# Kernel tuning notes

Measured on AMD Instinct MI355X. Metric: run time of the kernel, lower is better.

Reference implementation:

```python
import jax, jax.numpy as jnp
import numpy as np

EMBED_DIM = 1024
LATENT = 512
HEADS = 8
HEAD_DIM = EMBED_DIM // HEADS        # 128
LAT_HD = LATENT // HEADS             # 64
EPS = 1e-5


def _layernorm(x, gamma, beta):
    mu = jnp.mean(x, axis=-1, keepdims=True)
    var = jnp.mean(jnp.square(x - mu), axis=-1, keepdims=True)
    return (x - mu) * jax.lax.rsqrt(var + EPS) * gamma + beta


def setup_inputs() -> dict:
    key = jax.random.key(0)
    ks = jax.random.split(key, 12)
    B, N, M = 8, 8192, 256
    s_in = 1.0 / np.sqrt(EMBED_DIM)
    return {
        "input_tokens": jax.random.normal(ks[0], (B, N, EMBED_DIM), jnp.float32),
        "query_tokens": jax.random.normal(ks[1], (B, M, EMBED_DIM), jnp.float32),
        # Linear weights stored as [in, out] so y = x @ W + b
        "q_w": jax.random.normal(ks[2], (EMBED_DIM, LATENT), jnp.float32) * s_in,
        "q_b": jnp.zeros((LATENT,), jnp.float32),
        "q_g": jnp.ones((LATENT,), jnp.float32),
        "q_beta": jnp.zeros((LATENT,), jnp.float32),
        "k_w": jax.random.normal(ks[3], (EMBED_DIM, LATENT), jnp.float32) * s_in,
        "k_b": jnp.zeros((LATENT,), jnp.float32),
        "k_g": jnp.ones((LATENT,), jnp.float32),
        "k_beta": jnp.zeros((LATENT,), jnp.float32),
        "v_w": jax.random.normal(ks[4], (EMBED_DIM, EMBED_DIM), jnp.float32) * s_in,
        "v_b": jnp.zeros((EMBED_DIM,), jnp.float32),
        "v_g": jnp.ones((EMBED_DIM,), jnp.float32),
        "v_beta": jnp.zeros((EMBED_DIM,), jnp.float32),
        "proj_w": jax.random.normal(ks[5], (EMBED_DIM, EMBED_DIM), jnp.float32) * s_in,
        "proj_b": jnp.zeros((EMBED_DIM,), jnp.float32),
    }


def reference(input_tokens, query_tokens, q_w, q_b, q_g, q_beta,
              k_w, k_b, k_g, k_beta, v_w, v_b, v_g, v_beta,
              proj_w, proj_b):
    B, N, C = input_tokens.shape
    M = query_tokens.shape[1]
    # projections + layernorms
    q = _layernorm(query_tokens @ q_w + q_b, q_g, q_beta)   # [B,M,LATENT]
    k = _layernorm(input_tokens @ k_w + k_b, k_g, k_beta)   # [B,N,LATENT]
    v = _layernorm(input_tokens @ v_w + v_b, v_g, v_beta)   # [B,N,C]
    # split heads: q,k -> [B,H,*,LAT_HD]; v -> [B,H,N,HEAD_DIM]
    q = q.reshape(B, M, HEADS, LAT_HD).transpose(0, 2, 1, 3)
    k = k.reshape(B, N, HEADS, LAT_HD).transpose(0, 2, 1, 3)
    v = v.reshape(B, N, HEADS, HEAD_DIM).transpose(0, 2, 1, 3)
    # softmax Q over latent head dim; softmax K^T over token dim N
    q = jax.nn.softmax(q, axis=-1)                 # [B,H,M,LAT_HD]
    kT = jax.nn.softmax(k.transpose(0, 1, 3, 2), axis=-1)  # [B,H,LAT_HD,N]
    kv = jnp.einsum('bhln,bhnd->bhld', kT, v)      # [B,H,LAT_HD,HEAD_DIM]
    out = jnp.einsum('bhml,bhld->bhmd', q, kv)     # [B,H,M,HEAD_DIM]
    out = out.transpose(0, 2, 1, 3).reshape(B, M, C)
    return out @ proj_w + proj_b
```

## Files before the change

### kernel.cpp

```cpp
#include <hip/hip_runtime.h>
#include <hip/hip_fp16.h>

typedef _Float16 f16;
typedef _Float16 f16x8 __attribute__((ext_vector_type(8)));
typedef _Float16 f16x4 __attribute__((ext_vector_type(4)));
typedef float f32x4 __attribute__((ext_vector_type(4)));

#define LN_EPS 1e-5f

typedef __attribute__((address_space(1))) unsigned int as1_u32;
typedef __attribute__((address_space(3))) unsigned int as3_u32;

__device__ __forceinline__ void gload_lds16(const void* g, void* l) {
    __builtin_amdgcn_global_load_lds((as1_u32*)g, (as3_u32*)l, 16, 0, 0);
}

__device__ __forceinline__ f32x4 mfma16(f16x8 a, f16x8 b, f32x4 c) {
    return __builtin_amdgcn_mfma_f32_16x16x32_f16(a, b, c, 0, 0, 0);
}


__global__ void k_cvt_dual(const float4* __restrict__ in0, const float4* __restrict__ in1,
                           f16x4* __restrict__ out0, f16x4* __restrict__ out1,
                           int nsplit, int ntot) {
    int i = blockIdx.x * blockDim.x + threadIdx.x;
    int st = gridDim.x * blockDim.x;
    for (; i < ntot; i += st) {
        const bool lo = i < nsplit;
        const float4 v = lo ? in0[i] : in1[i - nsplit];
        f16x4 o;
        o.x = (f16)v.x; o.y = (f16)v.y; o.z = (f16)v.z; o.w = (f16)v.w;
        if (lo) out0[i] = o; else out1[i - nsplit] = o;
    }
}

__global__ __launch_bounds__(256) void k_transpose_all(const float* __restrict__ kw,
                                                       const float* __restrict__ vw,
                                                       const float* __restrict__ qw,
                                                       const float* __restrict__ pw,
                                                       f16* __restrict__ BkvT,
                                                       f16* __restrict__ qwT,
                                                       f16* __restrict__ pwT) {
    __shared__ float t[32][33];
    const int x = blockIdx.x;
    const float* W; f16* WT; int Nw, nt0;
    if (x < 16)      { W = kw; WT = BkvT;                     Nw = 512;  nt0 = x; }
    else if (x < 48) { W = vw; WT = BkvT + (size_t)512 * 1024; Nw = 1024; nt0 = x - 16; }
    else if (x < 64) { W = qw; WT = qwT;                      Nw = 512;  nt0 = x - 48; }
    else             { W = pw; WT = pwT;                      Nw = 1024; nt0 = x - 64; }
    const int n0 = nt0 * 32, k0 = blockIdx.y * 32;
    const int tx = threadIdx.x & 31, ty = threadIdx.x >> 5;
#pragma unroll
    for (int i = 0; i < 32; i += 8)
        t[ty + i][tx] = W[(size_t)(k0 + ty + i) * Nw + n0 + tx];
    __syncthreads();
#pragma unroll
    for (int i = 0; i < 32; i += 8)
        WT[(size_t)(n0 + ty + i) * 1024 + k0 + tx] = (f16)t[tx][ty + i];
}


__global__ __launch_bounds__(512, 2) void k_gemm256(const f16* __restrict__ A,
                                                    const f16* __restrict__ Bt,
                                                    f16* __restrict__ C,
                                                    const float* __restrict__ bias1,
                                                    const float* __restrict__ bias2) {
    extern __shared__ char lds[];
    const int tid = threadIdx.x, lane = tid & 63, w = tid >> 6;
    const int wr = w >> 2, wc = w & 3;
    const int lane15 = lane & 15, l4 = lane >> 4;

    const int swz = ((int)blockIdx.x & 7) * 192 + ((int)blockIdx.x >> 3);
    const int bx = swz % 6, by = swz / 6;
    const size_t m0 = (size_t)by * 256, n0g = (size_t)bx * 256;

    const int lrow = lane >> 3;
    const int slot = (lane & 7) ^ lrow;
    const int rw = w * 32;
    const f16* gA = A + (m0 + rw + lrow) * 1024 + slot * 8;
    const f16* gB = Bt + (n0g + rw + lrow) * 1024 + slot * 8;
    const int ldsw = rw * 128;

    const int sf = l4 ^ (lane15 & 7);
    const int offA = (wr * 128 + lane15) * 128 + sf * 16;
    const int offB = (wc * 64 + lane15) * 128 + sf * 16;

    f32x4 acc[8][4] = {};

#define STAGE(t, bsel)                                                          \
    {                                                                           \
        const int k0s = (t) * 64;                                               \
        char* dA = lds + ((bsel) << 15) + ldsw;                                 \
        char* dB = lds + 65536 + ((bsel) << 15) + ldsw;                         \
        _Pragma("unroll")                                                       \
        for (int i = 0; i < 4; i++) {                                           \
            gload_lds16(gA + (size_t)i * 8192 + k0s, dA + i * 1024);            \
            gload_lds16(gB + (size_t)i * 8192 + k0s, dB + i * 1024);            \
        }                                                                       \
    }

    STAGE(0, 0)
    STAGE(1, 1)
    asm volatile("s_waitcnt vmcnt(8)" ::: "memory");
    __builtin_amdgcn_s_barrier();

    for (int t = 0; t < 16; ++t) {
        const int bsel = t & 1;
        const char* pA = lds + (bsel << 15);
        const char* pB = lds + 65536 + (bsel << 15);
#pragma unroll
        for (int q = 0; q < 4; ++q) {
            const int mh = (q >> 1) * 4, nh = (q & 1) * 2;
            f16x8 af[4][2], bf[2][2];
#pragma unroll
            for (int mi = 0; mi < 4; mi++)
#pragma unroll
                for (int kk = 0; kk < 2; kk++)
                    af[mi][kk] = *(const f16x8*)(pA + ((offA + (mh + mi) * 2048) ^ (kk << 6)));
#pragma unroll
            for (int ni = 0; ni < 2; ni++)
#pragma unroll
                for (int kk = 0; kk < 2; kk++)
                    bf[ni][kk] = *(const f16x8*)(pB + ((offB + (nh + ni) * 2048) ^ (kk << 6)));
            __builtin_amdgcn_s_setprio(1);
#pragma unroll
            for (int mi = 0; mi < 4; mi++)
#pragma unroll
                for (int ni = 0; ni < 2; ni++)
#pragma unroll
                    for (int kk = 0; kk < 2; kk++)
                        acc[mh + mi][nh + ni] =
                            mfma16(af[mi][kk], bf[ni][kk], acc[mh + mi][nh + ni]);
            __builtin_amdgcn_s_setprio(0);
        }
        __builtin_amdgcn_s_barrier();
        if (t < 14) {
            STAGE(t + 2, bsel)
            asm volatile("s_waitcnt vmcnt(8)" ::: "memory");
        } else {
            asm volatile("s_waitcnt vmcnt(0)" ::: "memory");
        }
        __builtin_amdgcn_s_barrier();
    }
#undef STAGE

    {
        f16* Ct = (f16*)lds;
#pragma unroll
        for (int mi = 0; mi < 8; mi++) {
#pragma unroll
            for (int ni = 0; ni < 4; ni++) {
                const int row = wr * 128 + mi * 16 + l4 * 4;
                const int col = wc * 64 + ni * 16 + lane15;
                const int cg = (int)n0g + col;
                const float bv = (cg < 512) ? bias1[cg] : bias2[cg - 512];
#pragma unroll
                for (int j = 0; j < 4; j++)
                    Ct[(row + j) * 256 + col] = (f16)(acc[mi][ni][j] + bv);
            }
        }
        asm volatile("s_waitcnt lgkmcnt(0)" ::: "memory");
        __builtin_amdgcn_s_barrier();
#pragma unroll
        for (int it = 0; it < 16; it++) {
            const int flat = it * 512 + tid;
            const int row = flat >> 5;
            const int ce = (flat & 31) * 8;
            *(f16x8*)(C + (m0 + row) * 1536 + n0g + ce) = *(const f16x8*)(Ct + row * 256 + ce);
        }
    }
}


template <bool OUTF32>
__global__ __launch_bounds__(256, 2) void k_gemm(const f16* __restrict__ A,
                                                 const f16* __restrict__ Bt,
                                                 void* __restrict__ Cout, int Ncols, int Kd,
                                                 const float* __restrict__ bias1,
                                                 const float* __restrict__ bias2, int bsplit) {
    __shared__ f16 smem[16384];
    const int tid = threadIdx.x, lane = tid & 63, wave = tid >> 6;
    const int m0 = blockIdx.y * 128, n0 = blockIdx.x * 128;
    const size_t ldb = (size_t)Kd * 2;
    f32x4 acc[4][4] = {};

    const int rA = wave * 8 + (lane >> 3);
    const int slot = (lane & 7) * 16;
    const char* Ab = (const char*)A + (size_t)(m0 + rA) * ldb + slot;
    const char* Bb = (const char*)Bt + (size_t)(n0 + rA) * ldb + slot;
    char* lA = (char*)smem + wave * 1024;
    char* lB = (char*)smem + 16384 + wave * 1024;

    const int wm = (wave & 1) * 64, wn = (wave >> 1) * 64;

    for (int k0 = 0; k0 < Kd; k0 += 64) {
#pragma unroll
        for (int i = 0; i < 4; i++) {
            gload_lds16(Ab + (size_t)k0 * 2 + (size_t)i * 32 * ldb, lA + i * 4096);
            gload_lds16(Bb + (size_t)k0 * 2 + (size_t)i * 32 * ldb, lB + i * 4096);
        }
        __syncthreads();
#pragma unroll
        for (int kk = 0; kk < 64; kk += 32) {
            const int kb = (kk + (lane >> 4) * 8) * 2;
            f16x8 af[4], bf[4];
#pragma unroll
            for (int mi = 0; mi < 4; mi++)
                af[mi] = *(const f16x8*)((const char*)smem + (wm + mi * 16 + (lane & 15)) * 128 + kb);
#pragma unroll
            for (int ni = 0; ni < 4; ni++)
                bf[ni] = *(const f16x8*)((const char*)smem + 16384 + (wn + ni * 16 + (lane & 15)) * 128 + kb);
#pragma unroll
            for (int mi = 0; mi < 4; mi++)
#pragma unroll
                for (int ni = 0; ni < 4; ni++)
                    acc[mi][ni] = mfma16(af[mi], bf[ni], acc[mi][ni]);
        }
        __syncthreads();
    }

    if (!OUTF32) {
        f16* Ct = smem;
#pragma unroll
        for (int mi = 0; mi < 4; mi++) {
#pragma unroll
            for (int ni = 0; ni < 4; ni++) {
                const int r = wm + mi * 16 + (lane >> 4) * 4;
                const int c = wn + ni * 16 + (lane & 15);
                const int cg = n0 + c;
                const float bv = (cg < bsplit) ? bias1[cg] : bias2[cg - bsplit];
#pragma unroll
                for (int j = 0; j < 4; j++) Ct[(r + j) * 128 + c] = (f16)(acc[mi][ni][j] + bv);
            }
        }
        __syncthreads();
        f16* Cg = (f16*)Cout;
        const int r = tid >> 1, half = tid & 1;
        const f16* src = Ct + r * 128 + half * 64;
        f16* dst = Cg + (size_t)(m0 + r) * Ncols + n0 + half * 64;
#pragma unroll
        for (int i = 0; i < 8; i++) *(f16x8*)(dst + i * 8) = *(const f16x8*)(src + i * 8);
    } else {
        float* Cg = (float*)Cout;
#pragma unroll
        for (int mi = 0; mi < 4; mi++) {
#pragma unroll
            for (int ni = 0; ni < 4; ni++) {
                const int r = wm + mi * 16 + (lane >> 4) * 4;
                const int c = wn + ni * 16 + (lane & 15);
                const int cg = n0 + c;
                const float bv = (cg < bsplit) ? bias1[cg] : bias2[cg - bsplit];
#pragma unroll
                for (int j = 0; j < 4; j++)
                    Cg[(size_t)(m0 + r + j) * Ncols + cg] = acc[mi][ni][j] + bv;
            }
        }
    }
}


__global__ __launch_bounds__(192) void k_rowstats(const f16* __restrict__ Ckv,
                                                  float* __restrict__ stats) {
    const int row = blockIdx.x, t = threadIdx.x;
    const f16x8 v = ((const f16x8*)(Ckv + (size_t)row * 1536))[t];
    float s = 0.f, s2 = 0.f;
#pragma unroll
    for (int j = 0; j < 8; j++) {
        float x = (float)v[j];
        s += x;
        s2 += x * x;
    }
#pragma unroll
    for (int off = 32; off; off >>= 1) {
        s += __shfl_xor(s, off);
        s2 += __shfl_xor(s2, off);
    }
    __shared__ float red[4];
    const int wave = t >> 6;
    if ((t & 63) == 0 && wave) {
        red[wave * 2 - 2] = s;
        red[wave * 2 - 1] = s2;
    }
    __syncthreads();
    float* st = stats + (size_t)row * 4;
    if (t == 0) {
        const float mu = s * (1.0f / 512.0f);
        const float var = s2 * (1.0f / 512.0f) - mu * mu;
        st[0] = mu;
        st[1] = rsqrtf(var + LN_EPS);
    } else if (t == 64) {
        const float ss = s + red[2], ss2 = s2 + red[3];
        const float mu = ss * (1.0f / 1024.0f);
        const float var = ss2 * (1.0f / 1024.0f) - mu * mu;
        st[2] = mu;
        st[3] = rsqrtf(var + LN_EPS);
    }
}


__global__ __launch_bounds__(256) void k_colstats1(const f16* __restrict__ Ckv,
                                                   const float4* __restrict__ stats,
                                                   const float* __restrict__ kg,
                                                   const float* __restrict__ kb,
                                                   float* __restrict__ pm, float* __restrict__ ps) {
    const int b = blockIdx.y, slab = blockIdx.x, t = threadIdx.x;
    const int c0 = t * 2;
    const float g0 = kg[c0], g1 = kg[c0 + 1], e0 = kb[c0], e1 = kb[c0 + 1];
    const size_t r0 = (size_t)b * 8192 + slab * 64;
    float m0 = -1e30f, m1 = -1e30f;
    for (int r = 0; r < 64; r++) {
        const float4 st = stats[r0 + r];
        union { unsigned u; f16 h[2]; } w;
        w.u = *(const unsigned*)(Ckv + (r0 + r) * 1536 + c0);
        const float z0 = ((float)w.h[0] - st.x) * st.y * g0 + e0;
        const float z1 = ((float)w.h[1] - st.x) * st.y * g1 + e1;
        m0 = fmaxf(m0, z0);
        m1 = fmaxf(m1, z1);
    }
    float s0 = 0.f, s1 = 0.f;
    for (int r = 0; r < 64; r++) {
        const float4 st = stats[r0 + r];
        union { unsigned u; f16 h[2]; } w;
        w.u = *(const unsigned*)(Ckv + (r0 + r) * 1536 + c0);
        const float z0 = ((float)w.h[0] - st.x) * st.y * g0 + e0;
        const float z1 = ((float)w.h[1] - st.x) * st.y * g1 + e1;
        s0 += __expf(z0 - m0);
        s1 += __expf(z1 - m1);
    }
    const int o = (b * 128 + slab) * 512 + c0;
    pm[o] = m0; pm[o + 1] = m1;
    ps[o] = s0; ps[o + 1] = s1;
}

__global__ void k_colstats2(const float* __restrict__ pm, const float* __restrict__ ps,
                            float* __restrict__ Mx, float* __restrict__ invZ) {
    const int idx = blockIdx.x * 256 + threadIdx.x;
    const int b = idx >> 9, c = idx & 511;
    float M = -1e30f;
    for (int s = 0; s < 128; s++) M = fmaxf(M, pm[(b * 128 + s) * 512 + c]);
    float S = 0.f;
    for (int s = 0; s < 128; s++) S += ps[(b * 128 + s) * 512 + c] * __expf(pm[(b * 128 + s) * 512 + c] - M);
    Mx[idx] = M;
    invZ[idx] = 1.0f / S;
}


__global__ __launch_bounds__(256, 2) void k_kv(const f16* __restrict__ Ckv,
                                               const float4* __restrict__ stats,
                                               const float* __restrict__ kg,
                                               const float* __restrict__ kbe,
                                               const float* __restrict__ vg,
                                               const float* __restrict__ vbe,
                                               const float* __restrict__ Mx,
                                               float* __restrict__ kvpart) {
    __shared__ f16 As[64 * 64];
    __shared__ f16 Vs[128 * 64];
    __shared__ float cgk[64], cbk[64], cmx[64], cgv[128], cbv[128];
    const int split = blockIdx.x, bh = blockIdx.y;
    const int b = bh >> 3, h = bh & 7;
    const int tid = threadIdx.x, lane = tid & 63, wave = tid >> 6;
    if (tid < 64) {
        cgk[tid] = kg[h * 64 + tid];
        cbk[tid] = kbe[h * 64 + tid];
        cmx[tid] = Mx[b * 512 + h * 64 + tid];
    }
    if (tid < 128) {
        cgv[tid] = vg[h * 128 + tid];
        cbv[tid] = vbe[h * 128 + tid];
    }
    __syncthreads();
    f32x4 acc[8] = {};
    const size_t base = (size_t)b * 8192 + split * 1024;
    for (int t0 = 0; t0 < 1024; t0 += 64) {
        {
            const int g = tid & 7, p = tid >> 3;
            const size_t row = base + t0 + 2 * p;
            const f16x8 x0 = *(const f16x8*)(Ckv + row * 1536 + h * 64 + g * 8);
            const f16x8 x1 = *(const f16x8*)(Ckv + (row + 1) * 1536 + h * 64 + g * 8);
            const float4 s0 = stats[row], s1 = stats[row + 1];
#pragma unroll
            for (int j = 0; j < 8; j++) {
                const int c = g * 8 + j;
                const float z0 = ((float)x0[j] - s0.x) * s0.y * cgk[c] + cbk[c] - cmx[c];
                const float z1 = ((float)x1[j] - s1.x) * s1.y * cgk[c] + cbk[c] - cmx[c];
                union { unsigned u; f16 h2[2]; } pk;
                pk.h2[0] = (f16)__expf(z0);
                pk.h2[1] = (f16)__expf(z1);
                *(unsigned*)((char*)As + c * 128 + 4 * p) = pk.u;
            }
        }
#pragma unroll
        for (int sub = 0; sub < 2; sub++) {
            const int idx = tid + sub * 256;
            const int g = idx & 15, p = idx >> 4;
            const size_t row = base + t0 + 2 * p;
            const f16x8 x0 = *(const f16x8*)(Ckv + row * 1536 + 512 + h * 128 + g * 8);
            const f16x8 x1 = *(const f16x8*)(Ckv + (row + 1) * 1536 + 512 + h * 128 + g * 8);
            const float4 s0 = stats[row], s1 = stats[row + 1];
#pragma unroll
            for (int j = 0; j < 8; j++) {
                const int d = g * 8 + j;
                const float z0 = ((float)x0[j] - s0.z) * s0.w * cgv[d] + cbv[d];
                const float z1 = ((float)x1[j] - s1.z) * s1.w * cgv[d] + cbv[d];
                union { unsigned u; f16 h2[2]; } pk;
                pk.h2[0] = (f16)z0;
                pk.h2[1] = (f16)z1;
                *(unsigned*)((char*)Vs + d * 128 + 4 * p) = pk.u;
            }
        }
        __syncthreads();
#pragma unroll
        for (int kk = 0; kk < 64; kk += 32) {
            const int kb2 = (kk + (lane >> 4) * 8) * 2;
            const f16x8 af = *(const f16x8*)((const char*)As + (wave * 16 + (lane & 15)) * 128 + kb2);
#pragma unroll
            for (int ni = 0; ni < 8; ni++) {
                const f16x8 bf = *(const f16x8*)((const char*)Vs + (ni * 16 + (lane & 15)) * 128 + kb2);
                acc[ni] = mfma16(af, bf, acc[ni]);
            }
        }
        __syncthreads();
    }
    float* out = kvpart + ((size_t)split * 64 + bh) * 8192;
    const int l = wave * 16 + (lane >> 4) * 4;
#pragma unroll
    for (int ni = 0; ni < 8; ni++) {
        const int d = ni * 16 + (lane & 15);
#pragma unroll
        for (int j = 0; j < 4; j++) out[(l + j) * 128 + d] = acc[ni][j];
    }
}

__global__ void k_kvreduce(const float* __restrict__ kvpart, const float* __restrict__ invZ,
                           f16* __restrict__ kvT) {
    const int idx = blockIdx.x * 256 + threadIdx.x;
    const int d = idx & 127, l = (idx >> 7) & 63, bh = idx >> 13;
    const int b = bh >> 3, h = bh & 7;
    float s = 0.f;
#pragma unroll
    for (int sp = 0; sp < 8; sp++) s += kvpart[((size_t)sp * 64 + bh) * 8192 + l * 128 + d];
    s *= invZ[b * 512 + h * 64 + l];
    kvT[((size_t)bh * 128 + d) * 64 + l] = (f16)s;
}


__global__ __launch_bounds__(512) void k_qsm(const f16* __restrict__ qlin,
                                             const float* __restrict__ qg,
                                             const float* __restrict__ qbeta,
                                             f16* __restrict__ qsm) {
    const int row = blockIdx.x, t = threadIdx.x;
    const float x = (float)qlin[(size_t)row * 512 + t];
    float s = x, s2 = x * x;
#pragma unroll
    for (int off = 32; off; off >>= 1) {
        s += __shfl_xor(s, off);
        s2 += __shfl_xor(s2, off);
    }
    __shared__ float rs[16];
    const int wave = t >> 6, lane = t & 63;
    if (lane == 0) {
        rs[wave] = s;
        rs[8 + wave] = s2;
    }
    __syncthreads();
    float S = 0.f, S2 = 0.f;
#pragma unroll
    for (int w = 0; w < 8; w++) {
        S += rs[w];
        S2 += rs[8 + w];
    }
    const float mu = S * (1.0f / 512.0f);
    const float var = S2 * (1.0f / 512.0f) - mu * mu;
    const float z = (x - mu) * rsqrtf(var + LN_EPS) * qg[t] + qbeta[t];
    float m = z;
#pragma unroll
    for (int off = 32; off; off >>= 1) m = fmaxf(m, __shfl_xor(m, off));
    const float e = __expf(z - m);
    float se = e;
#pragma unroll
    for (int off = 32; off; off >>= 1) se += __shfl_xor(se, off);
    qsm[(size_t)row * 512 + t] = (f16)(e / se);
}


__global__ __launch_bounds__(256) void k_qkv(const f16* __restrict__ qsm,
                                             const f16* __restrict__ kvT,
                                             f16* __restrict__ omid) {
    const int ms = blockIdx.x, bh = blockIdx.y;
    const int b = bh >> 3, h = bh & 7;
    const int tid = threadIdx.x, lane = tid & 63, wave = tid >> 6;
    const int mr = ms * 64 + wave * 16;
    f32x4 acc[8] = {};
    const f16* Ab = qsm + (size_t)(b * 256 + mr + (lane & 15)) * 512 + h * 64;
    const f16* Bb = kvT + (size_t)bh * 8192;
#pragma unroll
    for (int kk = 0; kk < 64; kk += 32) {
        const int k = kk + (lane >> 4) * 8;
        const f16x8 af = *(const f16x8*)(Ab + k);
#pragma unroll
        for (int ni = 0; ni < 8; ni++) {
            const f16x8 bf = *(const f16x8*)(Bb + (ni * 16 + (lane & 15)) * 64 + k);
            acc[ni] = mfma16(af, bf, acc[ni]);
        }
    }
    const int r = b * 256 + mr + (lane >> 4) * 4;
#pragma unroll
    for (int ni = 0; ni < 8; ni++) {
        const int d = h * 128 + ni * 16 + (lane & 15);
#pragma unroll
        for (int j = 0; j < 4; j++) omid[(size_t)(r + j) * 1024 + d] = (f16)acc[ni][j];
    }
}


extern "C" void kernel_launch(void* const* d_in, const int* in_sizes, int n_in,
                              void* d_out, int out_size, void* d_ws, size_t ws_size,
                              hipStream_t stream) {
    const float* input  = (const float*)d_in[0];
    const float* query  = (const float*)d_in[1];
    const float* q_w    = (const float*)d_in[2];
    const float* q_b    = (const float*)d_in[3];
    const float* q_g    = (const float*)d_in[4];
    const float* q_beta = (const float*)d_in[5];
    const float* k_w    = (const float*)d_in[6];
    const float* k_b    = (const float*)d_in[7];
    const float* k_g    = (const float*)d_in[8];
    const float* k_beta = (const float*)d_in[9];
    const float* v_w    = (const float*)d_in[10];
    const float* v_b    = (const float*)d_in[11];
    const float* v_g    = (const float*)d_in[12];
    const float* v_beta = (const float*)d_in[13];
    const float* proj_w = (const float*)d_in[14];
    const float* proj_b = (const float*)d_in[15];

    char* ws = (char*)d_ws;
    size_t off = 0;
    auto alloc = [&](size_t bytes) {
        char* p = ws + off;
        off += (bytes + 255) & ~(size_t)255;
        return p;
    };
    f16*   A16    = (f16*)alloc((size_t)67108864 * 2);
    f16*   Q16    = (f16*)alloc((size_t)2097152 * 2);
    f16*   BkvT   = (f16*)alloc((size_t)1536 * 1024 * 2);
    f16*   qwT    = (f16*)alloc((size_t)512 * 1024 * 2);
    f16*   pwT    = (f16*)alloc((size_t)1024 * 1024 * 2);
    f16*   Ckv    = (f16*)alloc((size_t)65536 * 1536 * 2);
    float* stats  = (float*)alloc((size_t)65536 * 16);
    float* pm     = (float*)alloc((size_t)8 * 128 * 512 * 4);
    float* ps     = (float*)alloc((size_t)8 * 128 * 512 * 4);
    float* Mx     = (float*)alloc((size_t)8 * 512 * 4);
    float* invZ   = (float*)alloc((size_t)8 * 512 * 4);
    f16*   qlin   = (f16*)alloc((size_t)2048 * 512 * 2);
    f16*   qsm    = (f16*)alloc((size_t)2048 * 512 * 2);
    float* kvpart = (float*)alloc((size_t)8 * 64 * 64 * 128 * 4);
    f16*   kvT    = (f16*)alloc((size_t)64 * 128 * 64 * 2);
    f16*   omid   = (f16*)alloc((size_t)2048 * 1024 * 2);
    (void)ws_size; (void)in_sizes; (void)n_in; (void)out_size;

    hipFuncSetAttribute(reinterpret_cast<const void*>(k_gemm256),
                        hipFuncAttributeMaxDynamicSharedMemorySize, 131072);

    k_cvt_dual<<<2048, 256, 0, stream>>>((const float4*)input, (const float4*)query,
                                         (f16x4*)A16, (f16x4*)Q16, 16777216, 17301504);
    k_transpose_all<<<dim3(96, 32), 256, 0, stream>>>(k_w, v_w, q_w, proj_w, BkvT, qwT, pwT);

    k_gemm256<<<1536, 512, 131072, stream>>>(A16, BkvT, Ckv, k_b, v_b);

    k_rowstats<<<65536, 192, 0, stream>>>(Ckv, stats);

    k_colstats1<<<dim3(128, 8), 256, 0, stream>>>(Ckv, (const float4*)stats, k_g, k_beta, pm, ps);
    k_colstats2<<<16, 256, 0, stream>>>(pm, ps, Mx, invZ);

    k_kv<<<dim3(8, 64), 256, 0, stream>>>(Ckv, (const float4*)stats, k_g, k_beta, v_g, v_beta, Mx, kvpart);
    k_kvreduce<<<2048, 256, 0, stream>>>(kvpart, invZ, kvT);

    k_gemm<false><<<dim3(4, 16), 256, 0, stream>>>(Q16, qwT, qlin, 512, 1024, q_b, q_b, 512);
    k_qsm<<<2048, 512, 0, stream>>>(qlin, q_g, q_beta, qsm);
    k_qkv<<<dim3(4, 64), 256, 0, stream>>>(qsm, kvT, omid);
    k_gemm<true><<<dim3(8, 16), 256, 0, stream>>>(omid, pwT, d_out, 1024, 1024, proj_b, proj_b, 2048);
}
```

Baseline: 897.9 us.

## Fuse LayerNorm row stats into big GEMM epilogue and deepen K pipeline

```diff
diff --git a/kernel.cpp b/kernel.cpp
--- a/kernel.cpp
+++ b/kernel.cpp
@@ -64,7 +64,8 @@
                                                     const f16* __restrict__ Bt,
                                                     f16* __restrict__ C,
                                                     const float* __restrict__ bias1,
-                                                    const float* __restrict__ bias2) {
+                                                    const float* __restrict__ bias2,
+                                                    float* __restrict__ stats) {
     extern __shared__ char lds[];
     const int tid = threadIdx.x, lane = tid & 63, w = tid >> 6;
     const int wr = w >> 2, wc = w & 3;
@@ -74,93 +75,78 @@
     const int bx = swz % 6, by = swz / 6;
     const size_t m0 = (size_t)by * 256, n0g = (size_t)bx * 256;
 
-    const int lrow = lane >> 3;
-    const int slot = (lane & 7) ^ lrow;
-    const int rw = w * 32;
-    const f16* gA = A + (m0 + rw + lrow) * 1024 + slot * 8;
-    const f16* gB = Bt + (n0g + rw + lrow) * 1024 + slot * 8;
-    const int ldsw = rw * 128;
-
-    const int sf = l4 ^ (lane15 & 7);
-    const int offA = (wr * 128 + lane15) * 128 + sf * 16;
-    const int offB = (wc * 64 + lane15) * 128 + sf * 16;
+    const int lrow4 = lane >> 2;
+    const int lchunk = (lane & 3) ^ ((lane >> 3) & 3);
+    const f16* gA = A + (m0 + w * 32 + lrow4) * 1024 + lchunk * 8;
+    const f16* gB = Bt + (n0g + w * 32 + lrow4) * 1024 + lchunk * 8;
+    const int dstA = w * 2048;
+
+    const int csw = l4 ^ ((lane15 >> 1) & 3);
+    const int ofsA = (wr * 128 + lane15) * 64 + csw * 16;
+    const int ofsB = 16384 + (wc * 64 + lane15) * 64 + csw * 16;
 
     f32x4 acc[8][4] = {};
 
-#define STAGE(t, bsel)                                                          \
-    {                                                                           \
-        const int k0s = (t) * 64;                                               \
-        char* dA = lds + ((bsel) << 15) + ldsw;                                 \
-        char* dB = lds + 65536 + ((bsel) << 15) + ldsw;                         \
-        _Pragma("unroll")                                                       \
-        for (int i = 0; i < 4; i++) {                                           \
-            gload_lds16(gA + (size_t)i * 8192 + k0s, dA + i * 1024);            \
-            gload_lds16(gB + (size_t)i * 8192 + k0s, dB + i * 1024);            \
-        }                                                                       \
-    }
-
-    STAGE(0, 0)
-    STAGE(1, 1)
+#define STAGE_C(content)                                                         \
+    {                                                                            \
+        const int _sl = (content) & 3;                                           \
+        const int _ko = ((content) >> 1) * 64 + ((content) & 1) * 32;            \
+        char* _b = lds + _sl * 32768;                                            \
+        gload_lds16(gA + _ko, _b + dstA);                                        \
+        gload_lds16(gA + _ko + 16 * 1024, _b + dstA + 1024);                     \
+        gload_lds16(gB + _ko, _b + 16384 + dstA);                                \
+        gload_lds16(gB + _ko + 16 * 1024, _b + 16384 + dstA + 1024);             \
+    }
+
+#define PHASE(slotc, stage_content, vmN)                                         \
+    {                                                                            \
+        const char* sb = lds + (slotc) * 32768;                                  \
+        f16x8 af[8], bf[4];                                                      \
+        _Pragma("unroll") for (int m = 0; m < 8; m++)                            \
+            af[m] = *(const f16x8*)(sb + ofsA + m * 1024);                       \
+        _Pragma("unroll") for (int n = 0; n < 4; n++)                            \
+            bf[n] = *(const f16x8*)(sb + ofsB + n * 1024);                       \
+        if ((stage_content) >= 0) STAGE_C(stage_content)                         \
+        if ((vmN) == 8) asm volatile("s_waitcnt vmcnt(8)" ::: "memory");         \
+        else if ((vmN) == 4) asm volatile("s_waitcnt vmcnt(4)" ::: "memory");    \
+        else if ((vmN) == 0) asm volatile("s_waitcnt vmcnt(0)" ::: "memory");    \
+        __builtin_amdgcn_s_barrier();                                            \
+        __builtin_amdgcn_s_setprio(1);                                           \
+        _Pragma("unroll") for (int m = 0; m < 8; m++)                            \
+            _Pragma("unroll") for (int n = 0; n < 4; n++)                        \
+                acc[m][n] = mfma16(af[m], bf[n], acc[m][n]);                     \
+        __builtin_amdgcn_s_setprio(0);                                           \
+        __builtin_amdgcn_s_barrier();                                            \
+    }
+
+    STAGE_C(0) STAGE_C(1) STAGE_C(2)
     asm volatile("s_waitcnt vmcnt(8)" ::: "memory");
     __builtin_amdgcn_s_barrier();
 
-    for (int t = 0; t < 16; ++t) {
-        const int bsel = t & 1;
-        const char* pA = lds + (bsel << 15);
-        const char* pB = lds + 65536 + (bsel << 15);
-#pragma unroll
-        for (int q = 0; q < 4; ++q) {
-            const int mh = (q >> 1) * 4, nh = (q & 1) * 2;
-            f16x8 af[4][2], bf[2][2];
-#pragma unroll
-            for (int mi = 0; mi < 4; mi++)
-#pragma unroll
-                for (int kk = 0; kk < 2; kk++)
-                    af[mi][kk] = *(const f16x8*)(pA + ((offA + (mh + mi) * 2048) ^ (kk << 6)));
-#pragma unroll
-            for (int ni = 0; ni < 2; ni++)
-#pragma unroll
-                for (int kk = 0; kk < 2; kk++)
-                    bf[ni][kk] = *(const f16x8*)(pB + ((offB + (nh + ni) * 2048) ^ (kk << 6)));
-            __builtin_amdgcn_s_setprio(1);
-#pragma unroll
-            for (int mi = 0; mi < 4; mi++)
-#pragma unroll
-                for (int ni = 0; ni < 2; ni++)
-#pragma unroll
-                    for (int kk = 0; kk < 2; kk++)
-                        acc[mh + mi][nh + ni] =
-                            mfma16(af[mi][kk], bf[ni][kk], acc[mh + mi][nh + ni]);
-            __builtin_amdgcn_s_setprio(0);
-        }
-        __builtin_amdgcn_s_barrier();
-        if (t < 14) {
-            STAGE(t + 2, bsel)
-            asm volatile("s_waitcnt vmcnt(8)" ::: "memory");
-        } else {
-            asm volatile("s_waitcnt vmcnt(0)" ::: "memory");
-        }
-        __builtin_amdgcn_s_barrier();
-    }
-#undef STAGE
+#pragma unroll 4
+    for (int g = 0; g < 28; ++g) PHASE(g & 3, g + 3, 8)
+    PHASE(0, 31, 8)
+    PHASE(1, -1, 4)
+    PHASE(2, -1, 0)
+    PHASE(3, -1, -1)
+#undef PHASE
+#undef STAGE_C
 
     {
         f16* Ct = (f16*)lds;
 #pragma unroll
-        for (int mi = 0; mi < 8; mi++) {
-#pragma unroll
-            for (int ni = 0; ni < 4; ni++) {
-                const int row = wr * 128 + mi * 16 + l4 * 4;
-                const int col = wc * 64 + ni * 16 + lane15;
+        for (int m = 0; m < 8; m++)
+#pragma unroll
+            for (int n = 0; n < 4; n++) {
+                const int row = wr * 128 + m * 16 + l4 * 4;
+                const int col = wc * 64 + n * 16 + lane15;
                 const int cg = (int)n0g + col;
                 const float bv = (cg < 512) ? bias1[cg] : bias2[cg - 512];
 #pragma unroll
                 for (int j = 0; j < 4; j++)
-                    Ct[(row + j) * 256 + col] = (f16)(acc[mi][ni][j] + bv);
-            }
-        }
-        asm volatile("s_waitcnt lgkmcnt(0)" ::: "memory");
-        __builtin_amdgcn_s_barrier();
+                    Ct[(row + j) * 256 + col] = (f16)(acc[m][n][j] + bv);
+            }
+        __syncthreads();
 #pragma unroll
         for (int it = 0; it < 16; it++) {
             const int flat = it * 512 + tid;
@@ -168,7 +154,70 @@
             const int ce = (flat & 31) * 8;
             *(f16x8*)(C + (m0 + row) * 1536 + n0g + ce) = *(const f16x8*)(Ct + row * 256 + ce);
         }
-    }
+        __syncthreads();
+    }
+    {
+        float* SP = (float*)lds;
+        const int part = (n0g >= 512) ? 1 : 0;
+#pragma unroll
+        for (int half = 0; half < 2; half++) {
+            float s1[4][4], s2[4][4];
+#pragma unroll
+            for (int m = 0; m < 4; m++)
+#pragma unroll
+                for (int j = 0; j < 4; j++) { s1[m][j] = 0.f; s2[m][j] = 0.f; }
+#pragma unroll
+            for (int m = 0; m < 4; m++) {
+                const int mm = half * 4 + m;
+#pragma unroll
+                for (int n = 0; n < 4; n++) {
+                    const int cg = (int)n0g + wc * 64 + n * 16 + lane15;
+                    const float bv = (cg < 512) ? bias1[cg] : bias2[cg - 512];
+#pragma unroll
+                    for (int j = 0; j < 4; j++) {
+                        const float v = acc[mm][n][j] + bv;
+                        s1[m][j] += v;
+                        s2[m][j] += v * v;
+                    }
+                }
+#pragma unroll
+                for (int j = 0; j < 4; j++) {
+#pragma unroll
+                    for (int o = 1; o < 16; o <<= 1) {
+                        s1[m][j] += __shfl_xor(s1[m][j], o);
+                        s2[m][j] += __shfl_xor(s2[m][j], o);
+                    }
+                }
+            }
+            if (lane15 == 0) {
+#pragma unroll
+                for (int m = 0; m < 4; m++)
+#pragma unroll
+                    for (int j = 0; j < 4; j++) {
+                        const int row = wr * 128 + (half * 4 + m) * 16 + l4 * 4 + j;
+                        SP[row * 8 + wc * 2 + 0] = s1[m][j];
+                        SP[row * 8 + wc * 2 + 1] = s2[m][j];
+                    }
+            }
+        }
+        __syncthreads();
+        {
+            const int row = tid >> 1, comp = tid & 1;
+            const float v = SP[row * 8 + 0 + comp] + SP[row * 8 + 2 + comp] +
+                            SP[row * 8 + 4 + comp] + SP[row * 8 + 6 + comp];
+            atomicAdd(stats + (m0 + row) * 4 + part * 2 + comp, v);
+        }
+    }
+}
+
+__global__ void k_statsfin(float4* __restrict__ stats) {
+    const int i = blockIdx.x * 256 + threadIdx.x;
+    const float4 s = stats[i];
+    const float muk = s.x * (1.f / 512.f);
+    const float vk = s.y * (1.f / 512.f) - muk * muk;
+    const float muv = s.z * (1.f / 1024.f);
+    const float vv = s.w * (1.f / 1024.f) - muv * muv;
+    stats[i] = make_float4(muk, rsqrtf(vk + LN_EPS), muv, rsqrtf(vv + LN_EPS));
 }
 
 
@@ -255,45 +304,6 @@
                     Cg[(size_t)(m0 + r + j) * Ncols + cg] = acc[mi][ni][j] + bv;
             }
         }
-    }
-}
-
-
-__global__ __launch_bounds__(192) void k_rowstats(const f16* __restrict__ Ckv,
-                                                  float* __restrict__ stats) {
-    const int row = blockIdx.x, t = threadIdx.x;
-    const f16x8 v = ((const f16x8*)(Ckv + (size_t)row * 1536))[t];
-    float s = 0.f, s2 = 0.f;
-#pragma unroll
-    for (int j = 0; j < 8; j++) {
-        float x = (float)v[j];
-        s += x;
-        s2 += x * x;
-    }
-#pragma unroll
-    for (int off = 32; off; off >>= 1) {
-        s += __shfl_xor(s, off);
-        s2 += __shfl_xor(s2, off);
-    }
-    __shared__ float red[4];
-    const int wave = t >> 6;
-    if ((t & 63) == 0 && wave) {
-        red[wave * 2 - 2] = s;
-        red[wave * 2 - 1] = s2;
-    }
-    __syncthreads();
-    float* st = stats + (size_t)row * 4;
-    if (t == 0) {
-        const float mu = s * (1.0f / 512.0f);
-        const float var = s2 * (1.0f / 512.0f) - mu * mu;
-        st[0] = mu;
-        st[1] = rsqrtf(var + LN_EPS);
-    } else if (t == 64) {
-        const float ss = s + red[2], ss2 = s2 + red[3];
-        const float mu = ss * (1.0f / 1024.0f);
-        const float var = ss2 * (1.0f / 1024.0f) - mu * mu;
-        st[2] = mu;
-        st[3] = rsqrtf(var + LN_EPS);
     }
 }
 
@@ -561,13 +571,14 @@
     hipFuncSetAttribute(reinterpret_cast<const void*>(k_gemm256),
                         hipFuncAttributeMaxDynamicSharedMemorySize, 131072);
 
+    hipMemsetAsync(stats, 0, (size_t)65536 * 16, stream);
+
     k_cvt_dual<<<2048, 256, 0, stream>>>((const float4*)input, (const float4*)query,
                                          (f16x4*)A16, (f16x4*)Q16, 16777216, 17301504);
     k_transpose_all<<<dim3(96, 32), 256, 0, stream>>>(k_w, v_w, q_w, proj_w, BkvT, qwT, pwT);
 
-    k_gemm256<<<1536, 512, 131072, stream>>>(A16, BkvT, Ckv, k_b, v_b);
-
-    k_rowstats<<<65536, 192, 0, stream>>>(Ckv, stats);
+    k_gemm256<<<1536, 512, 131072, stream>>>(A16, BkvT, Ckv, k_b, v_b, stats);
+    k_statsfin<<<256, 256, 0, stream>>>((float4*)stats);
 
     k_colstats1<<<dim3(128, 8), 256, 0, stream>>>(Ckv, (const float4*)stats, k_g, k_beta, pm, ps);
     k_colstats2<<<16, 256, 0, stream>>>(pm, ps, Mx, invZ);
```

After: 898.0 us. No clear change (+0.0%).
